# Kernel optimization log

Hardware: AMD Instinct MI355X
Metric: run time of the kernel (lower is better)

Reference implementation:

```python
import jax, jax.numpy as jnp
import numpy as np

T, B, L = 8192, 8, 1024
HID, H, KV, D = 2048, 16, 8, 128
G = H // KV
EPS = 1e-6
SCALE = 1.0 / float(np.sqrt(D))


def _rms(x, w):
    # RMSNorm over last dim (head_dim), eps=1e-6
    return x * jax.lax.rsqrt(jnp.mean(x * x, axis=-1, keepdims=True) + EPS) * w


def _rot_half(x):
    h = x.shape[-1] // 2
    return jnp.concatenate([-x[..., h:], x[..., :h]], axis=-1)


def setup_inputs() -> dict:
    key = jax.random.key(0)
    ks = jax.random.split(key, 12)
    inp = {}
    inp["packed_sequence"] = jax.random.normal(ks[0], (T, HID), jnp.float32)
    # rotary embeddings: per-sample positions 0..L-1, packed
    pos = jnp.tile(jnp.arange(L), B).astype(jnp.float32)
    inv = 1.0 / (10000.0 ** (jnp.arange(0, D, 2, dtype=jnp.float32) / D))
    fr = pos[:, None] * inv[None, :]
    emb = jnp.concatenate([fr, fr], axis=-1)  # [T, D]
    inp["cos"] = jnp.cos(emb)
    inp["sin"] = jnp.sin(emb)
    # per-sample causal float mask (additive): 0 allowed, -1e9 masked
    tril = jnp.tril(jnp.ones((L, L), bool))
    inp["attention_mask"] = jnp.broadcast_to(
        jnp.where(tril, 0.0, -1e9).astype(jnp.float32)[None], (B, L, L)
    )
    # disjoint und/gen routing indexes covering all T tokens
    inp["und_idx"] = jnp.arange(0, T, 2, dtype=jnp.int32)
    inp["gen_idx"] = jnp.arange(1, T, 2, dtype=jnp.int32)
    s = 0.02

    def lin(k, o, i):
        return jax.random.normal(k, (o, i), jnp.float32) * s

    kk = jax.random.split(ks[1], 8)
    inp["Wq_u"] = lin(kk[0], H * D, HID); inp["bq_u"] = jnp.zeros((H * D,), jnp.float32)
    inp["Wk_u"] = lin(kk[1], KV * D, HID); inp["bk_u"] = jnp.zeros((KV * D,), jnp.float32)
    inp["Wv_u"] = lin(kk[2], KV * D, HID); inp["bv_u"] = jnp.zeros((KV * D,), jnp.float32)
    inp["Wo_u"] = lin(kk[3], HID, H * D)
    inp["Wq_g"] = lin(kk[4], H * D, HID); inp["bq_g"] = jnp.zeros((H * D,), jnp.float32)
    inp["Wk_g"] = lin(kk[5], KV * D, HID); inp["bk_g"] = jnp.zeros((KV * D,), jnp.float32)
    inp["Wv_g"] = lin(kk[6], KV * D, HID); inp["bv_g"] = jnp.zeros((KV * D,), jnp.float32)
    inp["Wo_g"] = lin(kk[7], HID, H * D)
    inp["qn_u"] = jnp.ones((D,), jnp.float32); inp["kn_u"] = jnp.ones((D,), jnp.float32)
    inp["qn_g"] = jnp.ones((D,), jnp.float32); inp["kn_g"] = jnp.ones((D,), jnp.float32)
    return inp


def reference(packed_sequence, cos, sin, attention_mask, und_idx, gen_idx,
              Wq_u, bq_u, Wk_u, bk_u, Wv_u, bv_u, Wo_u,
              Wq_g, bq_g, Wk_g, bk_g, Wv_g, bv_g, Wo_g,
              qn_u, kn_u, qn_g, kn_g):
    x_u = packed_sequence[und_idx]  # [T/2, HID]
    x_g = packed_sequence[gen_idx]

    def route(Wu, bu, Wg, bg, width):
        out = jnp.zeros((T, width), packed_sequence.dtype)
        out = out.at[und_idx].set(x_u @ Wu.T + bu)
        out = out.at[gen_idx].set(x_g @ Wg.T + bg)
        return out

    q = route(Wq_u, bq_u, Wq_g, bq_g, H * D).reshape(T, H, D)
    k = route(Wk_u, bk_u, Wk_g, bk_g, KV * D).reshape(T, KV, D)
    v = route(Wv_u, bv_u, Wv_g, bv_g, KV * D).reshape(T, KV, D)

    # routed per-head QK RMSNorm (separate und/gen weights)
    qn = jnp.zeros_like(q).at[und_idx].set(_rms(q[und_idx], qn_u)).at[gen_idx].set(_rms(q[gen_idx], qn_g))
    kn = jnp.zeros_like(k).at[und_idx].set(_rms(k[und_idx], kn_u)).at[gen_idx].set(_rms(k[gen_idx], kn_g))

    c, s = cos[:, None, :], sin[:, None, :]  # unsqueeze_dim=1
    q = qn * c + _rot_half(qn) * s
    k = kn * c + _rot_half(kn) * s

    # GQA expansion: kv head i -> heads i*G..i*G+G-1
    k = jnp.repeat(k, G, axis=1)  # [T, H, D]
    v = jnp.repeat(v, G, axis=1)

    qb = q.reshape(B, L, H, D)
    kb = k.reshape(B, L, H, D)
    vb = v.reshape(B, L, H, D)

    scores = jnp.einsum('blhd,bmhd->bhlm', qb, kb) * SCALE
    scores = scores + attention_mask[:, None, :, :]
    p = jax.nn.softmax(scores, axis=-1)
    o = jnp.einsum('bhlm,bmhd->blhd', p, vb).reshape(T, H * D)

    out = jnp.zeros((T, HID), packed_sequence.dtype)
    out = out.at[und_idx].set(o[und_idx] @ Wo_u.T)
    out = out.at[gen_idx].set(o[gen_idx] @ Wo_g.T)
    return out
```

## Files before the change

### kernel.cpp

```cpp
#include <hip/hip_runtime.h>
#include <hip/hip_bf16.h>
#include <stdint.h>
#include <math.h>

#define T_TOK 8192
#define HID   2048
#define NH    16
#define NKV   8
#define HD    128
#define LSEQ  1024
#define BATCH 8
#define QKV_N 4096
#define KDIM  2048
#define NTK   32
#define SCALE 0.08838834764831845f

typedef __hip_bfloat16 bf16;
typedef __bf16 bf16x8 __attribute__((ext_vector_type(8)));
typedef float  f32x4  __attribute__((ext_vector_type(4)));

typedef const void __attribute__((address_space(1)))* gas_ptr;
typedef void       __attribute__((address_space(3)))* las_ptr;

__device__ __forceinline__ float b2f(bf16 x) { return __bfloat162float(x); }
__device__ __forceinline__ bf16  f2b(float x) { return __float2bfloat16(x); }
__device__ __forceinline__ unsigned short f2u(float x) {
    union { bf16 b; unsigned short u; } c; c.b = __float2bfloat16(x); return c.u;
}

__device__ __forceinline__ bf16x8 ld16(const bf16* p) {
    union { uint4 u; bf16x8 v; } c;
    c.u = *reinterpret_cast<const uint4*>(p);
    return c.v;
}

__device__ __forceinline__ void cp16(void* lds, const void* g) {
    __builtin_amdgcn_global_load_lds((gas_ptr)g, (las_ptr)lds, 16, 0, 0);
}

__global__ __launch_bounds__(256) void k_f2b(const float* __restrict__ in,
                                             bf16* __restrict__ out, int n) {
    int i = blockIdx.x * blockDim.x + threadIdx.x;
    int stride = gridDim.x * blockDim.x;
    const float4* in4 = (const float4*)in;
    ushort4* out4 = (ushort4*)out;
    int n4 = n >> 2;
    for (int j = i; j < n4; j += stride) {
        float4 v = in4[j];
        ushort4 o;
        o.x = f2u(v.x); o.y = f2u(v.y); o.z = f2u(v.z); o.w = f2u(v.w);
        out4[j] = o;
    }
}

__global__ __launch_bounds__(256) void k_mod(const int* __restrict__ und,
                                             const int* __restrict__ gen,
                                             int* __restrict__ mod, int n) {
    int i = blockIdx.x * blockDim.x + threadIdx.x;
    if (i < n) { mod[und[i]] = 0; mod[gen[i]] = 1; }
}

template<int EPI>
__global__ __launch_bounds__(512)
void k_gemm256(const bf16* __restrict__ A,
               const bf16* __restrict__ Bw_u, const bf16* __restrict__ Bw_g,
               const int* __restrict__ und, const int* __restrict__ gen,
               const float* __restrict__ bq_u, const float* __restrict__ bk_u,
               const float* __restrict__ bv_u,
               const float* __restrict__ bq_g, const float* __restrict__ bk_g,
               const float* __restrict__ bv_g,
               bf16* __restrict__ outB, float* __restrict__ outF) {
    extern __shared__ char smem[];

    int modg = blockIdx.y;
    const bf16* Bw = modg ? Bw_g : Bw_u;
    const int* idx = modg ? gen : und;
    const float* bq = modg ? bq_g : bq_u;
    const float* bk = modg ? bk_g : bk_u;
    const float* bv = modg ? bv_g : bv_u;

    int gx = gridDim.x;
    int bid = blockIdx.x;
    int sw = (bid & 7) * (gx >> 3) + (bid >> 3);
    int tn = sw >> 4;
    int tm = sw & 15;

    int tid = threadIdx.x;
    int w = tid >> 6, lane = tid & 63;
    int l16 = lane & 15, l4 = lane >> 4;
    int wm = w >> 2, wn = w & 3;

    int srow = tid >> 3;
    int schunk = (tid & 7) ^ (srow & 7);
    const bf16* aSrc[4];
    const bf16* bSrc[4];
#pragma unroll
    for (int i = 0; i < 4; ++i) {
        int ar = tm * 256 + i * 64 + srow;
        aSrc[i] = A + (size_t)idx[ar] * KDIM + schunk * 8;
        bSrc[i] = Bw + (size_t)(tn * 256 + i * 64 + srow) * KDIM + schunk * 8;
    }

    auto STAGE = [&](int t) {
        char* Ab = smem + (t & 1) * 65536;
        char* Bb = Ab + 32768;
#pragma unroll
        for (int i = 0; i < 4; ++i) {
            cp16(Ab + i * 8192 + w * 1024, aSrc[i] + t * 64);
            cp16(Bb + i * 8192 + w * 1024, bSrc[i] + t * 64);
        }
    };

    f32x4 acc[8][4];
#pragma unroll
    for (int m = 0; m < 8; ++m)
#pragma unroll
        for (int n = 0; n < 4; ++n) acc[m][n] = {0.f, 0.f, 0.f, 0.f};

    STAGE(0);
    STAGE(1);

    uint32_t aRowByte = (uint32_t)(wm * 128 + l16) * 128;
    uint32_t bRowByte = (uint32_t)(wn * 64 + l16) * 128;
    uint32_t rx = (uint32_t)(l16 & 7);

#pragma unroll 1
    for (int t = 0; t < NTK; ++t) {
        if (t < NTK - 1) asm volatile("s_waitcnt vmcnt(8)" ::: "memory");
        else             asm volatile("s_waitcnt vmcnt(0)" ::: "memory");
        __builtin_amdgcn_s_barrier();
        asm volatile("" ::: "memory");

        const char* Ab = smem + (t & 1) * 65536;
        const char* Bb = Ab + 32768;
#pragma unroll
        for (int kk = 0; kk < 2; ++kk) {
            uint32_t cByte = ((((uint32_t)(kk << 2) | l4) ^ rx) << 4);
            bf16x8 af[8], bfr[4];
#pragma unroll
            for (int m = 0; m < 8; ++m)
                af[m] = ld16((const bf16*)(Ab + aRowByte + m * 2048 + cByte));
#pragma unroll
            for (int n = 0; n < 4; ++n)
                bfr[n] = ld16((const bf16*)(Bb + bRowByte + n * 2048 + cByte));
            __builtin_amdgcn_s_setprio(1);
#pragma unroll
            for (int m = 0; m < 8; ++m)
#pragma unroll
                for (int n = 0; n < 4; ++n)
                    acc[m][n] = __builtin_amdgcn_mfma_f32_16x16x32_bf16(af[m], bfr[n], acc[m][n], 0, 0, 0);
            __builtin_amdgcn_s_setprio(0);
        }

        asm volatile("" ::: "memory");
        __builtin_amdgcn_s_barrier();
        asm volatile("" ::: "memory");
        if (t + 2 < NTK) STAGE(t + 2);
    }

    int rowbase = tm * 256 + wm * 128;
    int colbase = tn * 256 + wn * 64;
#pragma unroll
    for (int m = 0; m < 8; ++m) {
#pragma unroll
        for (int r = 0; r < 4; ++r) {
            int row = rowbase + m * 16 + l4 * 4 + r;
            int token = idx[row];
#pragma unroll
            for (int n = 0; n < 4; ++n) {
                int col = colbase + n * 16 + l16;
                float v = acc[m][n][r];
                if (EPI == 0) {
                    float bias = (col < 2048) ? bq[col]
                               : (col < 3072) ? bk[col - 2048] : bv[col - 3072];
                    outB[(size_t)token * QKV_N + col] = f2b(v + bias);
                } else {
                    outF[(size_t)token * HID + col] = v;
                }
            }
        }
    }
}

__global__ __launch_bounds__(256)
void k_normrope(const bf16* __restrict__ qkv,
                const float* __restrict__ cosT, const float* __restrict__ sinT,
                const int* __restrict__ mod,
                const float* __restrict__ qn_u, const float* __restrict__ qn_g,
                const float* __restrict__ kn_u, const float* __restrict__ kn_g,
                bf16* __restrict__ Qo, bf16* __restrict__ Ko) {
    int t = blockIdx.x;
    int tid = threadIdx.x;
    int w = tid >> 6, lane = tid & 63;
    int m = mod[t];
    int b = t >> 10, pos = t & 1023;
    const bf16* row = qkv + (size_t)t * QKV_N;
    int d0 = 2 * lane, d1 = 2 * lane + 1;
    float c0 = cosT[(size_t)t * HD + d0], c1 = cosT[(size_t)t * HD + d1];
    float s0 = sinT[(size_t)t * HD + d0], s1 = sinT[(size_t)t * HD + d1];
    float sgn = (lane < 32) ? -1.f : 1.f;
    const float* qw = m ? qn_g : qn_u;
    const float* kw = m ? kn_g : kn_u;

    for (int u = w; u < 24; u += 4) {
        float v0 = b2f(row[u * HD + d0]);
        float v1 = b2f(row[u * HD + d1]);
        float ss = v0 * v0 + v1 * v1;
#pragma unroll
        for (int msk = 1; msk < 64; msk <<= 1) ss += __shfl_xor(ss, msk);
        float rs = rsqrtf(ss * (1.0f / HD) + 1e-6f);
        const float* wsc = (u < 16) ? qw : kw;
        float n0 = v0 * rs * wsc[d0], n1 = v1 * rs * wsc[d1];
        float o0 = __shfl_xor(n0, 32), o1 = __shfl_xor(n1, 32);
        float r0 = n0 * c0 + sgn * o0 * s0;
        float r1 = n1 * c1 + sgn * o1 * s1;
        if (u < 16) {
            size_t o = ((size_t)(b * NH + u) * LSEQ + pos) * HD;
            Qo[o + d0] = f2b(r0); Qo[o + d1] = f2b(r1);
        } else {
            size_t o = ((size_t)(b * NKV + (u - 16)) * LSEQ + pos) * HD;
            Ko[o + d0] = f2b(r0); Ko[o + d1] = f2b(r1);
        }
    }
}

__global__ __launch_bounds__(256)
void k_vt(const bf16* __restrict__ qkv, bf16* __restrict__ Vt) {
    __shared__ bf16 lds[64][72];
    int bk = blockIdx.x;
    int b = bk >> 3, kv = bk & 7;
    int pos0 = blockIdx.y * 64;
    int d0 = blockIdx.z * 64;
    int tid = threadIdx.x;

#pragma unroll
    for (int it = 0; it < 2; ++it) {
        int c = tid + it * 256;
        int row = c >> 3, col8 = (c & 7) * 8;
        const bf16* src = qkv + (size_t)(b * LSEQ + pos0 + row) * QKV_N
                        + 3072 + kv * HD + d0 + col8;
        *reinterpret_cast<uint4*>(&lds[row][col8]) = *reinterpret_cast<const uint4*>(src);
    }
    __syncthreads();

#pragma unroll
    for (int it = 0; it < 2; ++it) {
        int c = tid + it * 256;
        int drow = c & 63, pos8 = (c >> 6) * 8;
        union { unsigned short s[8]; uint4 u; } g;
#pragma unroll
        for (int j = 0; j < 8; ++j)
            g.s[j] = *reinterpret_cast<const unsigned short*>(&lds[pos8 + j][drow]);
        bf16* dst = Vt + ((size_t)bk * HD + d0 + drow) * LSEQ + pos0 + pos8;
        *reinterpret_cast<uint4*>(dst) = g.u;
    }
}

__global__ __launch_bounds__(256)
void k_attn(const bf16* __restrict__ Q, const bf16* __restrict__ K,
            const bf16* __restrict__ Vt, bf16* __restrict__ O) {
    int bid = blockIdx.x;
    int p = bid & 3;
    int h = (bid >> 2) & 15;
    int b = bid >> 6;
    int tid = threadIdx.x;
    int w = tid >> 6, lane = tid & 63;
    int l16 = lane & 15, l4 = lane >> 4;
    int j = p * 4 + w;

    const bf16* qhb = Q + (size_t)(b * NH + h) * LSEQ * HD;
    int kv = h >> 1;
    const bf16* kb = K + (size_t)(b * NKV + kv) * LSEQ * HD;
    const bf16* vtb = Vt + (size_t)(b * NKV + kv) * HD * LSEQ;

    __shared__ bf16 Pl[4][32][72];

    f32x4 zero = {0.f, 0.f, 0.f, 0.f};

#pragma unroll 1
    for (int half = 0; half < 2; ++half) {
        int rowblk = half ? (31 - j) : j;
        int q0 = rowblk * 32;
        int kend = q0 + 32;

        bf16x8 qf[2][4];
#pragma unroll
        for (int rf = 0; rf < 2; ++rf)
#pragma unroll
            for (int c = 0; c < 4; ++c)
                qf[rf][c] = ld16(qhb + (size_t)(q0 + rf * 16 + l16) * HD + c * 32 + l4 * 8);

        f32x4 oacc[2][8];
#pragma unroll
        for (int rf = 0; rf < 2; ++rf)
#pragma unroll
            for (int d = 0; d < 8; ++d) oacc[rf][d] = zero;
        float mr[2][4], lr[2][4];
#pragma unroll
        for (int rf = 0; rf < 2; ++rf)
#pragma unroll
            for (int r = 0; r < 4; ++r) { mr[rf][r] = -INFINITY; lr[rf][r] = 0.f; }

        for (int kt = 0; kt < kend; kt += 64) {
            f32x4 s[2][4];
#pragma unroll
            for (int rf = 0; rf < 2; ++rf)
#pragma unroll
                for (int kf = 0; kf < 4; ++kf) s[rf][kf] = zero;
#pragma unroll
            for (int c = 0; c < 4; ++c) {
                bf16x8 kf4[4];
#pragma unroll
                for (int kf = 0; kf < 4; ++kf)
                    kf4[kf] = ld16(kb + (size_t)(kt + kf * 16 + l16) * HD + c * 32 + l4 * 8);
#pragma unroll
                for (int rf = 0; rf < 2; ++rf)
#pragma unroll
                    for (int kf = 0; kf < 4; ++kf)
                        s[rf][kf] = __builtin_amdgcn_mfma_f32_16x16x32_bf16(qf[rf][c], kf4[kf], s[rf][kf], 0, 0, 0);
            }
#pragma unroll
            for (int rf = 0; rf < 2; ++rf) {
#pragma unroll
                for (int r = 0; r < 4; ++r) {
                    int qrow = q0 + rf * 16 + l4 * 4 + r;
                    float sc[4];
                    float rm = -1e30f;
#pragma unroll
                    for (int kf = 0; kf < 4; ++kf) {
                        int key = kt + kf * 16 + l16;
                        sc[kf] = (key <= qrow) ? s[rf][kf][r] * SCALE : -1e30f;
                        rm = fmaxf(rm, sc[kf]);
                    }
#pragma unroll
                    for (int msk = 1; msk < 16; msk <<= 1) rm = fmaxf(rm, __shfl_xor(rm, msk));
                    float mn = fmaxf(mr[rf][r], rm);
                    float corr = __expf(mr[rf][r] - mn);
                    mr[rf][r] = mn;
                    float rsum = 0.f;
#pragma unroll
                    for (int kf = 0; kf < 4; ++kf) {
                        float pv = __expf(sc[kf] - mn);
                        rsum += pv;
                        Pl[w][rf * 16 + l4 * 4 + r][kf * 16 + l16] = f2b(pv);
                    }
#pragma unroll
                    for (int msk = 1; msk < 16; msk <<= 1) rsum += __shfl_xor(rsum, msk);
                    lr[rf][r] = lr[rf][r] * corr + rsum;
#pragma unroll
                    for (int d = 0; d < 8; ++d) oacc[rf][d][r] *= corr;
                }
            }
            bf16x8 pf[2][2];
#pragma unroll
            for (int rf = 0; rf < 2; ++rf)
#pragma unroll
                for (int ks = 0; ks < 2; ++ks)
                    pf[rf][ks] = ld16(&Pl[w][rf * 16 + l16][ks * 32 + l4 * 8]);
#pragma unroll
            for (int dt = 0; dt < 8; ++dt) {
#pragma unroll
                for (int ks = 0; ks < 2; ++ks) {
                    bf16x8 vfr = ld16(vtb + (size_t)(dt * 16 + l16) * LSEQ + kt + ks * 32 + l4 * 8);
#pragma unroll
                    for (int rf = 0; rf < 2; ++rf)
                        oacc[rf][dt] = __builtin_amdgcn_mfma_f32_16x16x32_bf16(pf[rf][ks], vfr, oacc[rf][dt], 0, 0, 0);
                }
            }
        }

#pragma unroll
        for (int rf = 0; rf < 2; ++rf)
#pragma unroll
            for (int r = 0; r < 4; ++r) lr[rf][r] = 1.0f / lr[rf][r];
        int trow = b * LSEQ + q0;
#pragma unroll
        for (int rf = 0; rf < 2; ++rf)
#pragma unroll
            for (int dt = 0; dt < 8; ++dt)
#pragma unroll
                for (int r = 0; r < 4; ++r) {
                    int t = trow + rf * 16 + l4 * 4 + r;
                    O[(size_t)t * HID + h * HD + dt * 16 + l16] = f2b(oacc[rf][dt][r] * lr[rf][r]);
                }
    }
}

extern "C" void kernel_launch(void* const* d_in, const int* in_sizes, int n_in,
                              void* d_out, int out_size, void* d_ws, size_t ws_size,
                              hipStream_t stream) {
    const float* x    = (const float*)d_in[0];
    const float* cosT = (const float*)d_in[1];
    const float* sinT = (const float*)d_in[2];
    const int* und = (const int*)d_in[4];
    const int* gen = (const int*)d_in[5];
    const float* Wq_u = (const float*)d_in[6];
    const float* bq_u = (const float*)d_in[7];
    const float* Wk_u = (const float*)d_in[8];
    const float* bk_u = (const float*)d_in[9];
    const float* Wv_u = (const float*)d_in[10];
    const float* bv_u = (const float*)d_in[11];
    const float* Wo_u = (const float*)d_in[12];
    const float* Wq_g = (const float*)d_in[13];
    const float* bq_g = (const float*)d_in[14];
    const float* Wk_g = (const float*)d_in[15];
    const float* bk_g = (const float*)d_in[16];
    const float* Wv_g = (const float*)d_in[17];
    const float* bv_g = (const float*)d_in[18];
    const float* Wo_g = (const float*)d_in[19];
    const float* qn_u = (const float*)d_in[20];
    const float* kn_u = (const float*)d_in[21];
    const float* qn_g = (const float*)d_in[22];
    const float* kn_g = (const float*)d_in[23];
    float* out = (float*)d_out;

    char* ws = (char*)d_ws;
    size_t off = 0;
    auto alloc = [&](size_t bytes) -> void* {
        void* p = ws + off;
        off += (bytes + 255) & ~(size_t)255;
        return p;
    };
    bf16* xb      = (bf16*)alloc((size_t)T_TOK * HID * 2);
    bf16* Wqkv_u  = (bf16*)alloc((size_t)QKV_N * KDIM * 2);
    bf16* Wqkv_g  = (bf16*)alloc((size_t)QKV_N * KDIM * 2);
    bf16* Wob_u   = (bf16*)alloc((size_t)HID * HID * 2);
    bf16* Wob_g   = (bf16*)alloc((size_t)HID * HID * 2);
    int*  mod     = (int*)alloc((size_t)T_TOK * 4);
    bf16* qkv     = (bf16*)alloc((size_t)T_TOK * QKV_N * 2);
    bf16* Qa      = (bf16*)alloc((size_t)BATCH * NH  * LSEQ * HD * 2);
    bf16* Ka      = (bf16*)alloc((size_t)BATCH * NKV * LSEQ * HD * 2);
    bf16* Vt      = (bf16*)alloc((size_t)BATCH * NKV * HD * LSEQ * 2);
    bf16* Ob      = (bf16*)alloc((size_t)T_TOK * HID * 2);
    (void)ws_size; (void)in_sizes; (void)n_in; (void)out_size;

    (void)hipFuncSetAttribute((const void*)k_gemm256<0>,
                              hipFuncAttributeMaxDynamicSharedMemorySize, 131072);
    (void)hipFuncSetAttribute((const void*)k_gemm256<1>,
                              hipFuncAttributeMaxDynamicSharedMemorySize, 131072);

    k_f2b<<<1024, 256, 0, stream>>>(x, xb, T_TOK * HID);
    k_f2b<<<1024, 256, 0, stream>>>(Wq_u, Wqkv_u,               2048 * 2048);
    k_f2b<<<1024, 256, 0, stream>>>(Wk_u, Wqkv_u + 2048 * 2048, 1024 * 2048);
    k_f2b<<<1024, 256, 0, stream>>>(Wv_u, Wqkv_u + 3072 * 2048, 1024 * 2048);
    k_f2b<<<1024, 256, 0, stream>>>(Wq_g, Wqkv_g,               2048 * 2048);
    k_f2b<<<1024, 256, 0, stream>>>(Wk_g, Wqkv_g + 2048 * 2048, 1024 * 2048);
    k_f2b<<<1024, 256, 0, stream>>>(Wv_g, Wqkv_g + 3072 * 2048, 1024 * 2048);
    k_f2b<<<1024, 256, 0, stream>>>(Wo_u, Wob_u, 2048 * 2048);
    k_f2b<<<1024, 256, 0, stream>>>(Wo_g, Wob_g, 2048 * 2048);
    k_mod<<<16, 256, 0, stream>>>(und, gen, mod, T_TOK / 2);

    k_gemm256<0><<<dim3(16 * 16, 2), 512, 131072, stream>>>(
        xb, Wqkv_u, Wqkv_g, und, gen, bq_u, bk_u, bv_u, bq_g, bk_g, bv_g,
        qkv, nullptr);

    k_normrope<<<T_TOK, 256, 0, stream>>>(qkv, cosT, sinT, mod,
                                          qn_u, qn_g, kn_u, kn_g, Qa, Ka);
    k_vt<<<dim3(BATCH * NKV, LSEQ / 64, HD / 64), 256, 0, stream>>>(qkv, Vt);

    k_attn<<<BATCH * NH * 4, 256, 0, stream>>>(Qa, Ka, Vt, Ob);

    k_gemm256<1><<<dim3(8 * 16, 2), 512, 131072, stream>>>(
        Ob, Wob_u, Wob_g, und, gen, nullptr, nullptr, nullptr,
        nullptr, nullptr, nullptr, nullptr, out);
}
```

Before: 493.3 us.

## Restructure routed GEMM into 4-stage K=32 pipeline with split half-tile phases

The 256x256 routed GEMM kernel moves from a double-buffered K=64 loop to a four-deep ring of K=32 stages. Each iteration is split into two MFMA phases over the two halves of the M tile, with the next stage's A and B loads issued between them. The LDS swizzle is adjusted to the 64-byte row pitch. The goal is deeper prefetch and better overlap of global-to-LDS copies with MFMA work, at the cost of four barriers per iteration instead of two and twice as many iterations.

```diff
diff --git a/kernel.cpp b/kernel.cpp
--- a/kernel.cpp
+++ b/kernel.cpp
@@ -12,7 +12,7 @@
 #define BATCH 8
 #define QKV_N 4096
 #define KDIM  2048
-#define NTK   32
+#define NT32  64
 #define SCALE 0.08838834764831845f
 
 typedef __hip_bfloat16 bf16;
@@ -28,7 +28,7 @@
     union { bf16 b; unsigned short u; } c; c.b = __float2bfloat16(x); return c.u;
 }
 
-__device__ __forceinline__ bf16x8 ld16(const bf16* p) {
+__device__ __forceinline__ bf16x8 ld16(const void* p) {
     union { uint4 u; bf16x8 v; } c;
     c.u = *reinterpret_cast<const uint4*>(p);
     return c.v;
@@ -37,6 +37,10 @@
 __device__ __forceinline__ void cp16(void* lds, const void* g) {
     __builtin_amdgcn_global_load_lds((gas_ptr)g, (las_ptr)lds, 16, 0, 0);
 }
+
+#define BARX() do { asm volatile("" ::: "memory"); \
+                    __builtin_amdgcn_s_barrier();  \
+                    asm volatile("" ::: "memory"); } while (0)
 
 __global__ __launch_bounds__(256) void k_f2b(const float* __restrict__ in,
                                              bf16* __restrict__ out, int n) {
@@ -62,14 +66,14 @@
 
 template<int EPI>
 __global__ __launch_bounds__(512)
-void k_gemm256(const bf16* __restrict__ A,
-               const bf16* __restrict__ Bw_u, const bf16* __restrict__ Bw_g,
-               const int* __restrict__ und, const int* __restrict__ gen,
-               const float* __restrict__ bq_u, const float* __restrict__ bk_u,
-               const float* __restrict__ bv_u,
-               const float* __restrict__ bq_g, const float* __restrict__ bk_g,
-               const float* __restrict__ bv_g,
-               bf16* __restrict__ outB, float* __restrict__ outF) {
+void k_gemm8p(const bf16* __restrict__ A,
+              const bf16* __restrict__ Bw_u, const bf16* __restrict__ Bw_g,
+              const int* __restrict__ und, const int* __restrict__ gen,
+              const float* __restrict__ bq_u, const float* __restrict__ bk_u,
+              const float* __restrict__ bv_u,
+              const float* __restrict__ bq_g, const float* __restrict__ bk_g,
+              const float* __restrict__ bv_g,
+              bf16* __restrict__ outB, float* __restrict__ outF) {
     extern __shared__ char smem[];
 
     int modg = blockIdx.y;
@@ -82,80 +86,82 @@
     int gx = gridDim.x;
     int bid = blockIdx.x;
     int sw = (bid & 7) * (gx >> 3) + (bid >> 3);
-    int tn = sw >> 4;
-    int tm = sw & 15;
+    int tn = sw >> 4, tm = sw & 15;
 
     int tid = threadIdx.x;
     int w = tid >> 6, lane = tid & 63;
     int l16 = lane & 15, l4 = lane >> 4;
     int wm = w >> 2, wn = w & 3;
 
-    int srow = tid >> 3;
-    int schunk = (tid & 7) ^ (srow & 7);
-    const bf16* aSrc[4];
-    const bf16* bSrc[4];
-#pragma unroll
-    for (int i = 0; i < 4; ++i) {
-        int ar = tm * 256 + i * 64 + srow;
-        aSrc[i] = A + (size_t)idx[ar] * KDIM + schunk * 8;
-        bSrc[i] = Bw + (size_t)(tn * 256 + i * 64 + srow) * KDIM + schunk * 8;
-    }
-
-    auto STAGE = [&](int t) {
-        char* Ab = smem + (t & 1) * 65536;
-        char* Bb = Ab + 32768;
-#pragma unroll
-        for (int i = 0; i < 4; ++i) {
-            cp16(Ab + i * 8192 + w * 1024, aSrc[i] + t * 64);
-            cp16(Bb + i * 8192 + w * 1024, bSrc[i] + t * 64);
+    int chunk = (lane & 3) ^ ((lane >> 2) & 3);
+    const bf16* pS[2][2];
+#pragma unroll
+    for (int j = 0; j < 2; ++j) {
+        int R = (j * 8 + w) * 16 + (lane >> 2);
+        pS[0][j] = A + (size_t)idx[tm * 256 + R] * KDIM + chunk * 8;
+        pS[1][j] = Bw + (size_t)(tn * 256 + R) * KDIM + chunk * 8;
+    }
+
+    auto STAGE = [&](int t, int u) {
+        char* base = smem + (t & 3) * 32768 + u * 16384 + w * 1024;
+        cp16(base,        pS[u][0] + t * 32);
+        cp16(base + 8192, pS[u][1] + t * 32);
+    };
+
+    f32x4 acc[8][4];
+#pragma unroll
+    for (int m = 0; m < 8; ++m)
+#pragma unroll
+        for (int n = 0; n < 4; ++n) acc[m][n] = {0.f, 0.f, 0.f, 0.f};
+
+    STAGE(0, 0); STAGE(0, 1);
+    STAGE(1, 0); STAGE(1, 1);
+    STAGE(2, 0); STAGE(2, 1);
+    asm volatile("s_waitcnt vmcnt(8)" ::: "memory");
+    BARX();
+
+    uint32_t aRow = (uint32_t)(wm * 128 + l16) * 64;
+    uint32_t bRow = 16384u + (uint32_t)(wn * 64 + l16) * 64;
+    uint32_t cByte = (uint32_t)((l4 ^ (l16 & 3)) << 4);
+
+#pragma unroll 1
+    for (int t = 0; t < NT32; ++t) {
+        const char* buf = smem + (t & 3) * 32768;
+        bf16x8 bf_[4], af[4];
+#pragma unroll
+        for (int n = 0; n < 4; ++n) bf_[n] = ld16(buf + bRow + n * 1024 + cByte);
+#pragma unroll
+        for (int m = 0; m < 4; ++m) af[m] = ld16(buf + aRow + m * 1024 + cByte);
+        if (t + 3 < NT32) STAGE(t + 3, 0);
+        BARX();
+        __builtin_amdgcn_s_setprio(1);
+#pragma unroll
+        for (int m = 0; m < 4; ++m)
+#pragma unroll
+            for (int n = 0; n < 4; ++n)
+                acc[m][n] = __builtin_amdgcn_mfma_f32_16x16x32_bf16(af[m], bf_[n], acc[m][n], 0, 0, 0);
+        __builtin_amdgcn_s_setprio(0);
+        BARX();
+        bf16x8 af2[4];
+#pragma unroll
+        for (int m = 0; m < 4; ++m) af2[m] = ld16(buf + aRow + (m + 4) * 1024 + cByte);
+        if (t + 3 < NT32) {
+            STAGE(t + 3, 1);
+            asm volatile("s_waitcnt vmcnt(8)" ::: "memory");
+        } else if (t + 2 < NT32) {
+            asm volatile("s_waitcnt vmcnt(4)" ::: "memory");
+        } else {
+            asm volatile("s_waitcnt vmcnt(0)" ::: "memory");
         }
-    };
-
-    f32x4 acc[8][4];
-#pragma unroll
-    for (int m = 0; m < 8; ++m)
-#pragma unroll
-        for (int n = 0; n < 4; ++n) acc[m][n] = {0.f, 0.f, 0.f, 0.f};
-
-    STAGE(0);
-    STAGE(1);
-
-    uint32_t aRowByte = (uint32_t)(wm * 128 + l16) * 128;
-    uint32_t bRowByte = (uint32_t)(wn * 64 + l16) * 128;
-    uint32_t rx = (uint32_t)(l16 & 7);
-
-#pragma unroll 1
-    for (int t = 0; t < NTK; ++t) {
-        if (t < NTK - 1) asm volatile("s_waitcnt vmcnt(8)" ::: "memory");
-        else             asm volatile("s_waitcnt vmcnt(0)" ::: "memory");
-        __builtin_amdgcn_s_barrier();
-        asm volatile("" ::: "memory");
-
-        const char* Ab = smem + (t & 1) * 65536;
-        const char* Bb = Ab + 32768;
-#pragma unroll
-        for (int kk = 0; kk < 2; ++kk) {
-            uint32_t cByte = ((((uint32_t)(kk << 2) | l4) ^ rx) << 4);
-            bf16x8 af[8], bfr[4];
-#pragma unroll
-            for (int m = 0; m < 8; ++m)
-                af[m] = ld16((const bf16*)(Ab + aRowByte + m * 2048 + cByte));
+        BARX();
+        __builtin_amdgcn_s_setprio(1);
+#pragma unroll
+        for (int m = 0; m < 4; ++m)
 #pragma unroll
             for (int n = 0; n < 4; ++n)
-                bfr[n] = ld16((const bf16*)(Bb + bRowByte + n * 2048 + cByte));
-            __builtin_amdgcn_s_setprio(1);
-#pragma unroll
-            for (int m = 0; m < 8; ++m)
-#pragma unroll
-                for (int n = 0; n < 4; ++n)
-                    acc[m][n] = __builtin_amdgcn_mfma_f32_16x16x32_bf16(af[m], bfr[n], acc[m][n], 0, 0, 0);
-            __builtin_amdgcn_s_setprio(0);
-        }
-
-        asm volatile("" ::: "memory");
-        __builtin_amdgcn_s_barrier();
-        asm volatile("" ::: "memory");
-        if (t + 2 < NTK) STAGE(t + 2);
+                acc[m + 4][n] = __builtin_amdgcn_mfma_f32_16x16x32_bf16(af2[m], bf_[n], acc[m + 4][n], 0, 0, 0);
+        __builtin_amdgcn_s_setprio(0);
+        BARX();
     }
 
     int rowbase = tm * 256 + wm * 128;
@@ -434,9 +440,9 @@
     bf16* Ob      = (bf16*)alloc((size_t)T_TOK * HID * 2);
     (void)ws_size; (void)in_sizes; (void)n_in; (void)out_size;
 
-    (void)hipFuncSetAttribute((const void*)k_gemm256<0>,
+    (void)hipFuncSetAttribute((const void*)k_gemm8p<0>,
                               hipFuncAttributeMaxDynamicSharedMemorySize, 131072);
-    (void)hipFuncSetAttribute((const void*)k_gemm256<1>,
+    (void)hipFuncSetAttribute((const void*)k_gemm8p<1>,
                               hipFuncAttributeMaxDynamicSharedMemorySize, 131072);
 
     k_f2b<<<1024, 256, 0, stream>>>(x, xb, T_TOK * HID);
@@ -450,7 +456,7 @@
     k_f2b<<<1024, 256, 0, stream>>>(Wo_g, Wob_g, 2048 * 2048);
     k_mod<<<16, 256, 0, stream>>>(und, gen, mod, T_TOK / 2);
 
-    k_gemm256<0><<<dim3(16 * 16, 2), 512, 131072, stream>>>(
+    k_gemm8p<0><<<dim3(16 * 16, 2), 512, 131072, stream>>>(
         xb, Wqkv_u, Wqkv_g, und, gen, bq_u, bk_u, bv_u, bq_g, bk_g, bv_g,
         qkv, nullptr);
 
@@ -460,7 +466,7 @@
 
     k_attn<<<BATCH * NH * 4, 256, 0, stream>>>(Qa, Ka, Vt, Ob);
 
-    k_gemm256<1><<<dim3(8 * 16, 2), 512, 131072, stream>>>(
+    k_gemm8p<1><<<dim3(8 * 16, 2), 512, 131072, stream>>>(
         Ob, Wob_u, Wob_g, und, gen, nullptr, nullptr, nullptr,
         nullptr, nullptr, nullptr, nullptr, out);
 }
```

New measurement: 506.5 us. +2.7%, slower.
